# Optimization experiments

Hardware: AMD Instinct MI355X
Metric: run time of the kernel (lower is better)

## Reference

```python
import jax, jax.numpy as jnp
import numpy as np

NUM_HEADS = 8

def setup_inputs() -> dict:
    key = jax.random.key(0)
    ks = jax.random.split(key, 10)
    B, S, D = 4, 2048, 512
    scale = 1.0 / np.sqrt(D)
    return {
        "x": jax.random.normal(ks[0], (B, S, D), dtype=jnp.float32),
        "q": jax.random.normal(ks[1], (B, S, D), dtype=jnp.float32),
        "Wq": jax.random.normal(ks[2], (D, D), dtype=jnp.float32) * scale,
        "bq": jax.random.normal(ks[3], (D,), dtype=jnp.float32) * 0.01,
        "Wk": jax.random.normal(ks[4], (D, D), dtype=jnp.float32) * scale,
        "bk": jax.random.normal(ks[5], (D,), dtype=jnp.float32) * 0.01,
        "Wv": jax.random.normal(ks[6], (D, D), dtype=jnp.float32) * scale,
        "bv": jax.random.normal(ks[7], (D,), dtype=jnp.float32) * 0.01,
        "Wo": jax.random.normal(ks[8], (D, D), dtype=jnp.float32) * scale,
        "bo": jax.random.normal(ks[9], (D,), dtype=jnp.float32) * 0.01,
    }

def reference(x, q, Wq, bq, Wk, bk, Wv, bv, Wo, bo):
    B, S, D = x.shape
    H = NUM_HEADS
    Dh = D // H
    # Linear layers: y = x @ W.T + b (torch nn.Linear convention)
    def split_heads(t):  # [B,S,D] -> [B,H,S,Dh]
        return t.reshape(B, -1, H, Dh).transpose(0, 2, 1, 3)
    Q = split_heads(q @ Wq.T + bq)
    K = split_heads(x @ Wk.T + bk)
    V = split_heads(x @ Wv.T + bv)
    logits = jnp.einsum('bhqd,bhkd->bhqk', Q, K) / jnp.sqrt(jnp.asarray(Dh, Q.dtype))
    attn = jax.nn.softmax(logits, axis=-1)
    out = jnp.einsum('bhqk,bhkd->bhqd', attn, V)  # [B,H,S,Dh]
    concat = out.transpose(0, 2, 1, 3).reshape(B, -1, D)
    return concat @ Wo.T + bo
```

## Files before the change

kernel.cpp:

```cpp
#include <hip/hip_runtime.h>
#include <stdint.h>

typedef __bf16 bf16_t;
typedef bf16_t bf16x8 __attribute__((ext_vector_type(8)));
typedef bf16_t bf16x4 __attribute__((ext_vector_type(4)));
typedef bf16_t bf16x2 __attribute__((ext_vector_type(2)));
typedef float f32x4 __attribute__((ext_vector_type(4)));
typedef float f32x16 __attribute__((ext_vector_type(16)));
typedef uint32_t u32x4 __attribute__((ext_vector_type(4)));

#define DEV __device__ __forceinline__

DEV void gload_lds16(const void* g, void* l) {
  __builtin_amdgcn_global_load_lds(
      (__attribute__((address_space(1))) void*)(g),
      (__attribute__((address_space(3))) void*)(l), 16, 0, 0);
}

__global__ __launch_bounds__(256) void cvt_all_kernel(
    const float* __restrict__ x, const float* __restrict__ q,
    const float* __restrict__ Wq, const float* __restrict__ Wk,
    const float* __restrict__ Wv, const float* __restrict__ Wo,
    bf16_t* __restrict__ xb, bf16_t* __restrict__ qb, bf16_t* __restrict__ Wb) {
  const int y = blockIdx.y;
  int i = blockIdx.x * 256 + threadIdx.x;
  const float* s;
  bf16_t* d;
  if (y == 0) { s = x; d = xb; }
  else if (y == 1) { s = q; d = qb; }
  else {
    if (i >= 131072) return;
    int widx = i >> 15;
    s = (widx == 0) ? Wq : (widx == 1) ? Wk : (widx == 2) ? Wv : Wo;
    d = Wb + (size_t)widx * 262144;
    i &= 32767;
  }
  const float4* sp = (const float4*)s + (size_t)i * 2;
  float4 a = sp[0], b = sp[1];
  bf16x8 o;
  o[0] = (bf16_t)a.x; o[1] = (bf16_t)a.y; o[2] = (bf16_t)a.z; o[3] = (bf16_t)a.w;
  o[4] = (bf16_t)b.x; o[5] = (bf16_t)b.y; o[6] = (bf16_t)b.z; o[7] = (bf16_t)b.w;
  *(bf16x8*)(d + (size_t)i * 8) = o;
}

DEV void gemm_core(const bf16_t* __restrict__ A, const bf16_t* __restrict__ W,
                   char* smem, f32x4 (&acc)[4][4]) {
  const int tid = threadIdx.x;
  const int lane = tid & 63;
  const int wid = tid >> 6;
  const int wr = wid >> 1, wc = wid & 1;
  const int bx = blockIdx.x, by = blockIdx.y;

  uint32_t goffA[4], goffB[4], ldsoff[4];
#pragma unroll
  for (int c = 0; c < 4; ++c) {
    uint32_t o = (uint32_t)wid * 4096u + (uint32_t)c * 1024u + (uint32_t)lane * 16u;
    uint32_t row = o >> 7;
    uint32_t inner = (o & 127u) ^ ((row & 7u) << 4);
    goffA[c] = ((uint32_t)by * 128u + row) * 1024u + inner;
    goffB[c] = ((uint32_t)bx * 128u + row) * 1024u + inner;
    ldsoff[c] = o - (uint32_t)lane * 16u;
  }
  uint32_t offA[4][2], offB[4][2];
#pragma unroll
  for (int i = 0; i < 4; ++i)
#pragma unroll
    for (int kk = 0; kk < 2; ++kk) {
      uint32_t ra = (uint32_t)(wr * 64 + i * 16 + (lane & 15));
      offA[i][kk] = ra * 128u + (((uint32_t)kk * 64u + ((lane >> 4) * 16u)) ^ ((ra & 7u) << 4));
      uint32_t rb = (uint32_t)(wc * 64 + i * 16 + (lane & 15));
      offB[i][kk] = rb * 128u + (((uint32_t)kk * 64u + ((lane >> 4) * 16u)) ^ ((rb & 7u) << 4));
    }

  const char* Ab = (const char*)A;
  const char* Wb = (const char*)W;

#pragma unroll
  for (int c = 0; c < 4; ++c) {
    gload_lds16(Ab + goffA[c], smem + ldsoff[c]);
    gload_lds16(Wb + goffB[c], smem + 16384 + ldsoff[c]);
  }
  asm volatile("s_waitcnt vmcnt(0)" ::: "memory");
  __syncthreads();

#pragma unroll 1
  for (int kt = 0; kt < 8; ++kt) {
    const int buf = kt & 1;
    char* cur = smem + buf * 32768;
    if (kt < 7) {
      char* nxt = smem + (buf ^ 1) * 32768;
      uint32_t gk = (uint32_t)(kt + 1) * 128u;
#pragma unroll
      for (int c = 0; c < 4; ++c) {
        gload_lds16(Ab + goffA[c] + gk, nxt + ldsoff[c]);
        gload_lds16(Wb + goffB[c] + gk, nxt + 16384 + ldsoff[c]);
      }
    }
    bf16x8 af[4][2], bfr[4][2];
#pragma unroll
    for (int kk = 0; kk < 2; ++kk)
#pragma unroll
      for (int i = 0; i < 4; ++i) {
        af[i][kk] = *(const bf16x8*)(cur + offA[i][kk]);
        bfr[i][kk] = *(const bf16x8*)(cur + 16384 + offB[i][kk]);
      }
    __builtin_amdgcn_s_setprio(1);
#pragma unroll
    for (int kk = 0; kk < 2; ++kk)
#pragma unroll
      for (int mi = 0; mi < 4; ++mi)
#pragma unroll
        for (int nj = 0; nj < 4; ++nj)
          acc[mi][nj] = __builtin_amdgcn_mfma_f32_16x16x32_bf16(
              af[mi][kk], bfr[nj][kk], acc[mi][nj], 0, 0, 0);
    __builtin_amdgcn_s_setprio(0);
    asm volatile("s_waitcnt vmcnt(0)" ::: "memory");
    __syncthreads();
  }
}

__global__ __launch_bounds__(256) void gemm_qkv_kernel(
    const bf16_t* __restrict__ xb, const bf16_t* __restrict__ qb,
    const bf16_t* __restrict__ Wb, const float* __restrict__ bq,
    const float* __restrict__ bk, const float* __restrict__ bv,
    bf16_t* __restrict__ Qh, bf16_t* __restrict__ Kh, bf16_t* __restrict__ VT) {
  __shared__ char smem[65536];
  const int z = blockIdx.z;
  const bf16_t* A = (z == 0) ? qb : xb;
  const bf16_t* W = Wb + (size_t)z * 262144;
  const float* bias = (z == 0) ? bq : (z == 1) ? bk : bv;

  f32x4 acc[4][4] = {};
  gemm_core(A, W, smem, acc);

  const int lane = threadIdx.x & 63, wid = threadIdx.x >> 6;
  const int wr = wid >> 1, wc = wid & 1;
  const int colbase = blockIdx.x * 128 + wc * 64 + (lane & 15);
  const int rowbase = blockIdx.y * 128 + wr * 64 + ((lane >> 4) << 2);

  if (z == 2) {
#pragma unroll
    for (int nj = 0; nj < 4; ++nj) {
      int c = colbase + nj * 16;
      float bb = bias[c];
      int h = c >> 6, d = c & 63;
#pragma unroll
      for (int mi = 0; mi < 4; ++mi) {
        int r0 = rowbase + mi * 16;
        int b = r0 >> 11, s0 = r0 & 2047;
        bf16x4 v;
#pragma unroll
        for (int rr = 0; rr < 4; ++rr) v[rr] = (bf16_t)(acc[mi][nj][rr] + bb);
        *(bf16x4*)(VT + ((size_t)((b << 3) | h) * 64 + d) * 2048 + s0) = v;
      }
    }
  } else {
    bf16_t* O = (z == 0) ? Qh : Kh;
    const float scl = (z == 0) ? 0.18033688f : 1.0f;
#pragma unroll
    for (int nj = 0; nj < 4; ++nj) {
      int c = colbase + nj * 16;
      float bb = bias[c];
      int h = c >> 6, d = c & 63;
#pragma unroll
      for (int mi = 0; mi < 4; ++mi)
#pragma unroll
        for (int rr = 0; rr < 4; ++rr) {
          int r = rowbase + mi * 16 + rr;
          int b = r >> 11, s = r & 2047;
          O[((size_t)((b << 3) | h) * 2048 + s) * 64 + d] = (bf16_t)((acc[mi][nj][rr] + bb) * scl);
        }
    }
  }
}

__global__ __launch_bounds__(256) void gemm_out_kernel(
    const bf16_t* __restrict__ ctx, const bf16_t* __restrict__ Wo,
    const float* __restrict__ bo, float* __restrict__ out) {
  __shared__ char smem[65536];
  f32x4 acc[4][4] = {};
  gemm_core(ctx, Wo, smem, acc);

  const int lane = threadIdx.x & 63, wid = threadIdx.x >> 6;
  const int wr = wid >> 1, wc = wid & 1;
  const int colbase = blockIdx.x * 128 + wc * 64 + (lane & 15);
  const int rowbase = blockIdx.y * 128 + wr * 64 + ((lane >> 4) << 2);
#pragma unroll
  for (int nj = 0; nj < 4; ++nj) {
    int c = colbase + nj * 16;
    float bb = bo[c];
#pragma unroll
    for (int mi = 0; mi < 4; ++mi)
#pragma unroll
      for (int rr = 0; rr < 4; ++rr) {
        int r = rowbase + mi * 16 + rr;
        out[(size_t)r * 512 + c] = acc[mi][nj][rr] + bb;
      }
  }
}

__global__ __launch_bounds__(256, 2) void attn_kernel(
    const bf16_t* __restrict__ Qh, const bf16_t* __restrict__ Kh,
    const bf16_t* __restrict__ VT, bf16_t* __restrict__ ctx) {
  __shared__ char smem[65536];
  const int tid = threadIdx.x, lane = tid & 63, wid = tid >> 6;
  const int l31 = lane & 31, h = lane >> 5;
  const int bid = blockIdx.x + 16 * blockIdx.y;
  const int qt = (bid >> 3) & 15;
  const int bh = (bid & 7) * 4 + (bid >> 7);

  const char* Kbase = (const char*)Kh + (size_t)bh * 262144;
  const char* Vbase = (const char*)VT + (size_t)bh * 262144;
  const char* Qbase = (const char*)Qh + (size_t)bh * 262144;

  const int qrow = qt * 128 + wid * 32 + l31;
  bf16x8 qf[4];
#pragma unroll
  for (int ks = 0; ks < 4; ++ks)
    qf[ks] = *(const bf16x8*)(Qbase + (size_t)qrow * 128 + ks * 32 + h * 16);

  uint32_t kgo[2], vgo[2], lo[2];
#pragma unroll
  for (int c = 0; c < 2; ++c) {
    uint32_t o = (uint32_t)c * 4096u + (uint32_t)wid * 1024u + (uint32_t)lane * 16u;
    uint32_t row = o >> 7;
    uint32_t inner = (o & 127u) ^ ((row & 7u) << 4);
    kgo[c] = row * 128u + inner;
    vgo[c] = row * 4096u + inner;
    lo[c] = o - (uint32_t)lane * 16u;
  }

  const uint32_t swz = (uint32_t)(l31 & 7) << 4;
  uint32_t fbase[2], fcol[4];
#pragma unroll
  for (int c = 0; c < 2; ++c) fbase[c] = (uint32_t)(32 * c + l31) * 128u;
#pragma unroll
  for (int ks = 0; ks < 4; ++ks) fcol[ks] = ((uint32_t)(ks * 32 + h * 16)) ^ swz;

  f32x16 oacc[2] = {};
  float m_run = 0.0f, l_part = 0.f;

#pragma unroll
  for (int tt = 0; tt < 2; ++tt) {
    const char* Kt = Kbase + (size_t)tt * 8192;
    const char* Vt = Vbase + (size_t)tt * 128;
#pragma unroll
    for (int c = 0; c < 2; ++c) {
      gload_lds16(Kt + kgo[c], smem + tt * 8192 + lo[c]);
      gload_lds16(Vt + vgo[c], smem + 32768 + tt * 8192 + lo[c]);
    }
  }
  asm volatile("s_waitcnt vmcnt(0)" ::: "memory");
  __syncthreads();

#pragma unroll 1
  for (int te = 0; te < 16; ++te) {
    const int t0 = te * 2;
    if (t0 < 30) {
#pragma unroll
      for (int j = 2; j < 4; ++j) {
        const int tn = t0 + j;
        const uint32_t nb = ((uint32_t)tn & 3u) * 8192u;
        const char* Kn = Kbase + (size_t)tn * 8192;
        const char* Vn = Vbase + (size_t)tn * 128;
#pragma unroll
        for (int c = 0; c < 2; ++c) {
          gload_lds16(Kn + kgo[c], smem + nb + lo[c]);
          gload_lds16(Vn + vgo[c], smem + 32768 + nb + lo[c]);
        }
      }
    }

#pragma unroll
    for (int j = 0; j < 2; ++j) {
      const uint32_t cur = ((uint32_t)(t0 + j) & 3u) * 8192u;
      const char* Kc = smem + cur;
      const char* Vc = smem + 32768 + cur;

      f32x16 sT[2] = {};
#pragma unroll
      for (int c = 0; c < 2; ++c) {
        __builtin_amdgcn_s_setprio(1);
#pragma unroll
        for (int ks = 0; ks < 4; ++ks) {
          bf16x8 kf = *(const bf16x8*)(Kc + fbase[c] + fcol[ks]);
          sT[c] = __builtin_amdgcn_mfma_f32_32x32x16_bf16(kf, qf[ks], sT[c], 0, 0, 0);
        }
        __builtin_amdgcn_s_setprio(0);
      }

      uint32_t cw[2][8];
      float la0 = 0.f, la1 = 0.f, la2 = 0.f, la3 = 0.f;
#pragma unroll
      for (int c = 0; c < 2; ++c)
#pragma unroll
        for (int w = 0; w < 8; ++w) {
          float p0 = __builtin_exp2f(sT[c][2 * w] - m_run);
          float p1 = __builtin_exp2f(sT[c][2 * w + 1] - m_run);
          if ((w & 3) == 0) la0 += p0 + p1;
          else if ((w & 3) == 1) la1 += p0 + p1;
          else if ((w & 3) == 2) la2 += p0 + p1;
          else la3 += p0 + p1;
          bf16x2 tp; tp[0] = (bf16_t)p0; tp[1] = (bf16_t)p1;
          cw[c][w] = __builtin_bit_cast(uint32_t, tp);
        }
      float ladd = (la0 + la1) + (la2 + la3);
      if (!__all(ladd <= 16384.0f)) {
        float mx = sT[0][0];
#pragma unroll
        for (int c = 0; c < 2; ++c)
#pragma unroll
          for (int r = 0; r < 16; ++r) mx = fmaxf(mx, sT[c][r]);
        mx = fmaxf(mx, __shfl_xor(mx, 32));
        float mnew = fmaxf(m_run, mx);
        float sc = __builtin_exp2f(m_run - mnew);
        l_part *= sc;
#pragma unroll
        for (int r = 0; r < 16; ++r) { oacc[0][r] *= sc; oacc[1][r] *= sc; }
        m_run = mnew;
        la0 = la1 = la2 = la3 = 0.f;
#pragma unroll
        for (int c = 0; c < 2; ++c)
#pragma unroll
          for (int w = 0; w < 8; ++w) {
            float p0 = __builtin_exp2f(sT[c][2 * w] - m_run);
            float p1 = __builtin_exp2f(sT[c][2 * w + 1] - m_run);
            if ((w & 3) == 0) la0 += p0 + p1;
            else if ((w & 3) == 1) la1 += p0 + p1;
            else if ((w & 3) == 2) la2 += p0 + p1;
            else la3 += p0 + p1;
            bf16x2 tp; tp[0] = (bf16_t)p0; tp[1] = (bf16_t)p1;
            cw[c][w] = __builtin_bit_cast(uint32_t, tp);
          }
        ladd = (la0 + la1) + (la2 + la3);
      }
      l_part += ladd;

      bf16x8 pa[4];
#pragma unroll
      for (int s = 0; s < 4; ++s) {
        const int c = s >> 1, sp = s & 1;
        uint32_t w0 = cw[c][4 * sp + 0], w1 = cw[c][4 * sp + 1];
        uint32_t w2 = cw[c][4 * sp + 2], w3 = cw[c][4 * sp + 3];
        uint32_t snd0 = h ? w0 : w2;
        uint32_t snd1 = h ? w1 : w3;
        uint32_t rcv0 = (uint32_t)__shfl_xor((int)snd0, 32);
        uint32_t rcv1 = (uint32_t)__shfl_xor((int)snd1, 32);
        u32x4 ta;
        ta[0] = h ? rcv0 : w0;
        ta[1] = h ? rcv1 : w1;
        ta[2] = h ? w2 : rcv0;
        ta[3] = h ? w3 : rcv1;
        pa[s] = __builtin_bit_cast(bf16x8, ta);
      }

#pragma unroll
      for (int dc = 0; dc < 2; ++dc) {
        __builtin_amdgcn_s_setprio(1);
#pragma unroll
        for (int ks = 0; ks < 4; ++ks) {
          bf16x8 vf = *(const bf16x8*)(Vc + fbase[dc] + fcol[ks]);
          oacc[dc] = __builtin_amdgcn_mfma_f32_32x32x16_bf16(vf, pa[ks], oacc[dc], 0, 0, 0);
        }
        __builtin_amdgcn_s_setprio(0);
      }
    }

    asm volatile("s_waitcnt vmcnt(0)" ::: "memory");
    __syncthreads();
  }

  float l = l_part + __shfl_xor(l_part, 32);
  float inv = 1.0f / l;
  const int b = bh >> 3, hh = bh & 7;
  bf16_t* crow = ctx + ((size_t)(b * 2048 + qrow)) * 512 + hh * 64;
#pragma unroll
  for (int dc = 0; dc < 2; ++dc)
#pragma unroll
    for (int m = 0; m < 4; ++m) {
      bf16x4 v;
#pragma unroll
      for (int r = 0; r < 4; ++r) v[r] = (bf16_t)(oacc[dc][4 * m + r] * inv);
      *(bf16x4*)(crow + dc * 32 + m * 8 + h * 4) = v;
    }
}

extern "C" void kernel_launch(void* const* d_in, const int* in_sizes, int n_in,
                              void* d_out, int out_size, void* d_ws, size_t ws_size,
                              hipStream_t stream) {
  const float* x  = (const float*)d_in[0];
  const float* q  = (const float*)d_in[1];
  const float* Wq = (const float*)d_in[2];
  const float* bq = (const float*)d_in[3];
  const float* Wk = (const float*)d_in[4];
  const float* bk = (const float*)d_in[5];
  const float* Wv = (const float*)d_in[6];
  const float* bv = (const float*)d_in[7];
  const float* Wo = (const float*)d_in[8];
  const float* bo = (const float*)d_in[9];

  char* ws = (char*)d_ws;
  bf16_t* xb  = (bf16_t*)(ws + 0);
  bf16_t* qb  = (bf16_t*)(ws + 8388608);
  bf16_t* Wb  = (bf16_t*)(ws + 16777216);
  bf16_t* Qh  = (bf16_t*)(ws + 18874368);
  bf16_t* Kh  = (bf16_t*)(ws + 27262976);
  bf16_t* VT  = (bf16_t*)(ws + 35651584);
  bf16_t* ctx = (bf16_t*)(ws + 44040192);

  cvt_all_kernel<<<dim3(2048, 3), 256, 0, stream>>>(x, q, Wq, Wk, Wv, Wo, xb, qb, Wb);
  gemm_qkv_kernel<<<dim3(4, 64, 3), 256, 0, stream>>>(xb, qb, Wb, bq, bk, bv, Qh, Kh, VT);
  attn_kernel<<<dim3(16, 32), 256, 0, stream>>>(Qh, Kh, VT, ctx);
  gemm_out_kernel<<<dim3(4, 64), 256, 0, stream>>>(ctx, Wb + 3 * 262144, bo, (float*)d_out);
}
```

Measured before the change: 116.1 us.

## Software-pipeline attention loop so QK of next tile overlaps softmax/PV of current

Restructures the attention inner loop so the QK^T MFMAs for tile t+1 are issued before the softmax and PV work for tile t, using two score buffers (sA/sB). Loads are now issued one tile at a time, with a barrier after each tile instead of after each pair. The goal is to overlap matrix-core work with the exp/convert VALU work. The cost is higher register pressure from the extra live score accumulators and twice as many barriers.

```diff
diff --git a/kernel.cpp b/kernel.cpp
--- a/kernel.cpp
+++ b/kernel.cpp
@@ -199,6 +199,104 @@
   }
 }
 
+DEV void qk_tile(const char* Kc, const bf16x8 (&qf)[4],
+                 const uint32_t (&fbase)[2], const uint32_t (&fcol)[4],
+                 f32x16 (&sT)[2]) {
+  f32x16 s0 = {}, s1 = {};
+  __builtin_amdgcn_s_setprio(1);
+#pragma unroll
+  for (int ks = 0; ks < 4; ++ks) {
+    bf16x8 kf = *(const bf16x8*)(Kc + fbase[0] + fcol[ks]);
+    s0 = __builtin_amdgcn_mfma_f32_32x32x16_bf16(kf, qf[ks], s0, 0, 0, 0);
+  }
+#pragma unroll
+  for (int ks = 0; ks < 4; ++ks) {
+    bf16x8 kf = *(const bf16x8*)(Kc + fbase[1] + fcol[ks]);
+    s1 = __builtin_amdgcn_mfma_f32_32x32x16_bf16(kf, qf[ks], s1, 0, 0, 0);
+  }
+  __builtin_amdgcn_s_setprio(0);
+  sT[0] = s0; sT[1] = s1;
+}
+
+DEV void softmax_pv_tile(f32x16 (&sT)[2], const char* Vc, int h,
+                         const uint32_t (&fbase)[2], const uint32_t (&fcol)[4],
+                         f32x16 (&oacc)[2], float& m_run, float& l_part) {
+  uint32_t cw[2][8];
+  float la0 = 0.f, la1 = 0.f, la2 = 0.f, la3 = 0.f;
+#pragma unroll
+  for (int c = 0; c < 2; ++c)
+#pragma unroll
+    for (int w = 0; w < 8; ++w) {
+      float p0 = __builtin_exp2f(sT[c][2 * w] - m_run);
+      float p1 = __builtin_exp2f(sT[c][2 * w + 1] - m_run);
+      if ((w & 3) == 0) la0 += p0 + p1;
+      else if ((w & 3) == 1) la1 += p0 + p1;
+      else if ((w & 3) == 2) la2 += p0 + p1;
+      else la3 += p0 + p1;
+      bf16x2 tp; tp[0] = (bf16_t)p0; tp[1] = (bf16_t)p1;
+      cw[c][w] = __builtin_bit_cast(uint32_t, tp);
+    }
+  float ladd = (la0 + la1) + (la2 + la3);
+  if (!__all(ladd <= 16384.0f)) {
+    float mx = sT[0][0];
+#pragma unroll
+    for (int c = 0; c < 2; ++c)
+#pragma unroll
+      for (int r = 0; r < 16; ++r) mx = fmaxf(mx, sT[c][r]);
+    mx = fmaxf(mx, __shfl_xor(mx, 32));
+    float mnew = fmaxf(m_run, mx);
+    float sc = __builtin_exp2f(m_run - mnew);
+    l_part *= sc;
+#pragma unroll
+    for (int r = 0; r < 16; ++r) { oacc[0][r] *= sc; oacc[1][r] *= sc; }
+    m_run = mnew;
+    la0 = la1 = la2 = la3 = 0.f;
+#pragma unroll
+    for (int c = 0; c < 2; ++c)
+#pragma unroll
+      for (int w = 0; w < 8; ++w) {
+        float p0 = __builtin_exp2f(sT[c][2 * w] - m_run);
+        float p1 = __builtin_exp2f(sT[c][2 * w + 1] - m_run);
+        if ((w & 3) == 0) la0 += p0 + p1;
+        else if ((w & 3) == 1) la1 += p0 + p1;
+        else if ((w & 3) == 2) la2 += p0 + p1;
+        else la3 += p0 + p1;
+        bf16x2 tp; tp[0] = (bf16_t)p0; tp[1] = (bf16_t)p1;
+        cw[c][w] = __builtin_bit_cast(uint32_t, tp);
+      }
+    ladd = (la0 + la1) + (la2 + la3);
+  }
+  l_part += ladd;
+
+  bf16x8 pa[4];
+#pragma unroll
+  for (int s = 0; s < 4; ++s) {
+    const int c = s >> 1, sp = s & 1;
+    uint32_t w0 = cw[c][4 * sp + 0], w1 = cw[c][4 * sp + 1];
+    uint32_t w2 = cw[c][4 * sp + 2], w3 = cw[c][4 * sp + 3];
+    uint32_t snd0 = h ? w0 : w2;
+    uint32_t snd1 = h ? w1 : w3;
+    uint32_t rcv0 = (uint32_t)__shfl_xor((int)snd0, 32);
+    uint32_t rcv1 = (uint32_t)__shfl_xor((int)snd1, 32);
+    u32x4 ta;
+    ta[0] = h ? rcv0 : w0;
+    ta[1] = h ? rcv1 : w1;
+    ta[2] = h ? w2 : rcv0;
+    ta[3] = h ? w3 : rcv1;
+    pa[s] = __builtin_bit_cast(bf16x8, ta);
+  }
+
+  __builtin_amdgcn_s_setprio(1);
+#pragma unroll
+  for (int dc = 0; dc < 2; ++dc)
+#pragma unroll
+    for (int ks = 0; ks < 4; ++ks) {
+      bf16x8 vf = *(const bf16x8*)(Vc + fbase[dc] + fcol[ks]);
+      oacc[dc] = __builtin_amdgcn_mfma_f32_32x32x16_bf16(vf, pa[ks], oacc[dc], 0, 0, 0);
+    }
+  __builtin_amdgcn_s_setprio(0);
+}
+
 __global__ __launch_bounds__(256, 2) void attn_kernel(
     const bf16_t* __restrict__ Qh, const bf16_t* __restrict__ Kh,
     const bf16_t* __restrict__ VT, bf16_t* __restrict__ ctx) {
@@ -253,119 +351,42 @@
   asm volatile("s_waitcnt vmcnt(0)" ::: "memory");
   __syncthreads();
 
+  f32x16 sA[2], sB[2];
+  qk_tile(smem, qf, fbase, fcol, sA);
+
 #pragma unroll 1
   for (int te = 0; te < 16; ++te) {
-    const int t0 = te * 2;
-    if (t0 < 30) {
-#pragma unroll
-      for (int j = 2; j < 4; ++j) {
-        const int tn = t0 + j;
-        const uint32_t nb = ((uint32_t)tn & 3u) * 8192u;
-        const char* Kn = Kbase + (size_t)tn * 8192;
-        const char* Vn = Vbase + (size_t)tn * 128;
-#pragma unroll
-        for (int c = 0; c < 2; ++c) {
-          gload_lds16(Kn + kgo[c], smem + nb + lo[c]);
-          gload_lds16(Vn + vgo[c], smem + 32768 + nb + lo[c]);
-        }
-      }
-    }
-
-#pragma unroll
-    for (int j = 0; j < 2; ++j) {
-      const uint32_t cur = ((uint32_t)(t0 + j) & 3u) * 8192u;
-      const char* Kc = smem + cur;
-      const char* Vc = smem + 32768 + cur;
-
-      f32x16 sT[2] = {};
+    const int t0 = 2 * te, t1 = t0 + 1;
+
+    if (te < 15) {
+      const uint32_t nb = ((uint32_t)(t0 + 2) & 3u) * 8192u;
+      const char* Kn = Kbase + (size_t)(t0 + 2) * 8192;
+      const char* Vn = Vbase + (size_t)(t0 + 2) * 128;
 #pragma unroll
       for (int c = 0; c < 2; ++c) {
-        __builtin_amdgcn_s_setprio(1);
-#pragma unroll
-        for (int ks = 0; ks < 4; ++ks) {
-          bf16x8 kf = *(const bf16x8*)(Kc + fbase[c] + fcol[ks]);
-          sT[c] = __builtin_amdgcn_mfma_f32_32x32x16_bf16(kf, qf[ks], sT[c], 0, 0, 0);
-        }
-        __builtin_amdgcn_s_setprio(0);
-      }
-
-      uint32_t cw[2][8];
-      float la0 = 0.f, la1 = 0.f, la2 = 0.f, la3 = 0.f;
-#pragma unroll
-      for (int c = 0; c < 2; ++c)
-#pragma unroll
-        for (int w = 0; w < 8; ++w) {
-          float p0 = __builtin_exp2f(sT[c][2 * w] - m_run);
-          float p1 = __builtin_exp2f(sT[c][2 * w + 1] - m_run);
-          if ((w & 3) == 0) la0 += p0 + p1;
-          else if ((w & 3) == 1) la1 += p0 + p1;
-          else if ((w & 3) == 2) la2 += p0 + p1;
-          else la3 += p0 + p1;
-          bf16x2 tp; tp[0] = (bf16_t)p0; tp[1] = (bf16_t)p1;
-          cw[c][w] = __builtin_bit_cast(uint32_t, tp);
-        }
-      float ladd = (la0 + la1) + (la2 + la3);
-      if (!__all(ladd <= 16384.0f)) {
-        float mx = sT[0][0];
-#pragma unroll
-        for (int c = 0; c < 2; ++c)
-#pragma unroll
-          for (int r = 0; r < 16; ++r) mx = fmaxf(mx, sT[c][r]);
-        mx = fmaxf(mx, __shfl_xor(mx, 32));
-        float mnew = fmaxf(m_run, mx);
-        float sc = __builtin_exp2f(m_run - mnew);
-        l_part *= sc;
-#pragma unroll
-        for (int r = 0; r < 16; ++r) { oacc[0][r] *= sc; oacc[1][r] *= sc; }
-        m_run = mnew;
-        la0 = la1 = la2 = la3 = 0.f;
-#pragma unroll
-        for (int c = 0; c < 2; ++c)
-#pragma unroll
-          for (int w = 0; w < 8; ++w) {
-            float p0 = __builtin_exp2f(sT[c][2 * w] - m_run);
-            float p1 = __builtin_exp2f(sT[c][2 * w + 1] - m_run);
-            if ((w & 3) == 0) la0 += p0 + p1;
-            else if ((w & 3) == 1) la1 += p0 + p1;
-            else if ((w & 3) == 2) la2 += p0 + p1;
-            else la3 += p0 + p1;
-            bf16x2 tp; tp[0] = (bf16_t)p0; tp[1] = (bf16_t)p1;
-            cw[c][w] = __builtin_bit_cast(uint32_t, tp);
-          }
-        ladd = (la0 + la1) + (la2 + la3);
-      }
-      l_part += ladd;
-
-      bf16x8 pa[4];
-#pragma unroll
-      for (int s = 0; s < 4; ++s) {
-        const int c = s >> 1, sp = s & 1;
-        uint32_t w0 = cw[c][4 * sp + 0], w1 = cw[c][4 * sp + 1];
-        uint32_t w2 = cw[c][4 * sp + 2], w3 = cw[c][4 * sp + 3];
-        uint32_t snd0 = h ? w0 : w2;
-        uint32_t snd1 = h ? w1 : w3;
-        uint32_t rcv0 = (uint32_t)__shfl_xor((int)snd0, 32);
-        uint32_t rcv1 = (uint32_t)__shfl_xor((int)snd1, 32);
-        u32x4 ta;
-        ta[0] = h ? rcv0 : w0;
-        ta[1] = h ? rcv1 : w1;
-        ta[2] = h ? w2 : rcv0;
-        ta[3] = h ? w3 : rcv1;
-        pa[s] = __builtin_bit_cast(bf16x8, ta);
-      }
-
-#pragma unroll
-      for (int dc = 0; dc < 2; ++dc) {
-        __builtin_amdgcn_s_setprio(1);
-#pragma unroll
-        for (int ks = 0; ks < 4; ++ks) {
-          bf16x8 vf = *(const bf16x8*)(Vc + fbase[dc] + fcol[ks]);
-          oacc[dc] = __builtin_amdgcn_mfma_f32_32x32x16_bf16(vf, pa[ks], oacc[dc], 0, 0, 0);
-        }
-        __builtin_amdgcn_s_setprio(0);
-      }
-    }
-
+        gload_lds16(Kn + kgo[c], smem + nb + lo[c]);
+        gload_lds16(Vn + vgo[c], smem + 32768 + nb + lo[c]);
+      }
+    }
+    qk_tile(smem + ((uint32_t)t1 & 3u) * 8192u, qf, fbase, fcol, sB);
+    softmax_pv_tile(sA, smem + 32768 + ((uint32_t)t0 & 3u) * 8192u, h,
+                    fbase, fcol, oacc, m_run, l_part);
+    asm volatile("s_waitcnt vmcnt(0)" ::: "memory");
+    __syncthreads();
+
+    if (te < 15) {
+      const uint32_t nb = ((uint32_t)(t1 + 2) & 3u) * 8192u;
+      const char* Kn = Kbase + (size_t)(t1 + 2) * 8192;
+      const char* Vn = Vbase + (size_t)(t1 + 2) * 128;
+#pragma unroll
+      for (int c = 0; c < 2; ++c) {
+        gload_lds16(Kn + kgo[c], smem + nb + lo[c]);
+        gload_lds16(Vn + vgo[c], smem + 32768 + nb + lo[c]);
+      }
+      qk_tile(smem + ((uint32_t)(t1 + 1) & 3u) * 8192u, qf, fbase, fcol, sA);
+    }
+    softmax_pv_tile(sB, smem + 32768 + ((uint32_t)t1 & 3u) * 8192u, h,
+                    fbase, fcol, oacc, m_run, l_part);
     asm volatile("s_waitcnt vmcnt(0)" ::: "memory");
     __syncthreads();
   }
```

After: 126.0 us. 1.09x slower.
